# Performance work log

Hardware: AMD Instinct MI355X
Metric: run time of the kernel (lower is better)

## Reference

```python
import jax, jax.numpy as jnp
import numpy as np
import math

DIMS = [2048, 1024, 512, 4096]
NH, DK, DV = 16, 64, 64
BS = 8192
D_MODEL = NH * DK  # 1024


def setup_inputs() -> dict:
    key = jax.random.key(0)
    ks = jax.random.split(key, 3 * len(DIMS) + 5)
    inp = {"input_data": jax.random.normal(ks[0], (BS, sum(DIMS)), jnp.float32)}
    ki = 1
    for i, d in enumerate(DIMS):
        inp[f"wq{i}"] = jax.random.normal(ks[ki], (NH * DK, d), jnp.float32) * 0.02; ki += 1
        inp[f"wk{i}"] = jax.random.normal(ks[ki], (NH * DK, d), jnp.float32) * 0.02; ki += 1
        inp[f"wv{i}"] = jax.random.normal(ks[ki], (NH * DV, d), jnp.float32) * 0.02; ki += 1
    inp["fc_w"] = jax.random.normal(ks[ki], (NH * DV, NH * DV), jnp.float32) * 0.02; ki += 1
    inp["fc_b"] = jax.random.normal(ks[ki], (NH * DV,), jnp.float32) * 0.02; ki += 1
    inp["ln_g"] = jnp.ones((NH * DV,), jnp.float32)
    inp["ln_b"] = jnp.zeros((NH * DV,), jnp.float32)
    return inp


def _forward(input_data, wqs, wks, wvs, fc_w, fc_b, ln_g, ln_b):
    bs = input_data.shape[0]
    M = len(DIMS)
    offs = np.cumsum([0] + DIMS)
    # per-modality projections; stack into [bs, M, NH*D]
    xs = [input_data[:, offs[i]:offs[i + 1]] for i in range(M)]
    q = jnp.stack([x @ w.T for x, w in zip(xs, wqs)], axis=1)  # [bs, M, NH*DK]
    k = jnp.stack([x @ w.T for x, w in zip(xs, wks)], axis=1)
    v = jnp.stack([x @ w.T for x, w in zip(xs, wvs)], axis=1)  # [bs, M, NH*DV]
    residual = v  # v.transpose(1,2).view == original stacked v
    qh = q.reshape(bs, M, NH, DK).transpose(0, 2, 1, 3)  # [bs, NH, M, DK]
    kh = k.reshape(bs, M, NH, DK).transpose(0, 2, 1, 3)
    vh = v.reshape(bs, M, NH, DV).transpose(0, 2, 1, 3)
    scores = jnp.einsum('bhqd,bhkd->bhqk', qh, kh) / math.sqrt(DK)
    attn = jax.nn.softmax(scores, axis=-1)  # [bs, NH, M, M]
    ctx = jnp.einsum('bhqk,bhkd->bhqd', attn, vh)  # [bs, NH, M, DV]
    ctx = ctx.transpose(0, 2, 1, 3).reshape(bs, M, NH * DV)
    out = ctx @ fc_w.T + fc_b  # dropout is identity (p=0 / eval)
    out = out + residual
    mu = jnp.mean(out, axis=-1, keepdims=True)
    var = jnp.var(out, axis=-1, keepdims=True)
    out = (out - mu) / jnp.sqrt(var + 1e-6) * ln_g + ln_b
    return out, attn


def reference(input_data, wq0, wk0, wv0, wq1, wk1, wv1, wq2, wk2, wv2,
              wq3, wk3, wv3, fc_w, fc_b, ln_g, ln_b):
    wqs = [wq0, wq1, wq2, wq3]
    wks = [wk0, wk1, wk2, wk3]
    wvs = [wv0, wv1, wv2, wv3]
    return _forward(input_data, wqs, wks, wvs, fc_w, fc_b, ln_g, ln_b)
```

## Files before the change

### kernel.cpp

```cpp
#include <hip/hip_runtime.h>


typedef unsigned short u16;
typedef short short8 __attribute__((ext_vector_type(8)));
typedef float f32x4 __attribute__((ext_vector_type(4)));

__device__ __forceinline__ u16 f2bf(float f) {
  unsigned u = __builtin_bit_cast(unsigned, f);
  u += 0x7FFFu + ((u >> 16) & 1u);
  return (u16)(u >> 16);
}
__device__ __forceinline__ float bf2f(u16 s) {
  return __builtin_bit_cast(float, ((unsigned)s) << 16);
}

__device__ __forceinline__ void gload16(const u16* g, u16* l) {
  __builtin_amdgcn_global_load_lds(
      (const __attribute__((address_space(1))) void*)g,
      (__attribute__((address_space(3))) void*)l, 16, 0, 0);
}

#define CFENCE asm volatile("" ::: "memory")

struct CArgs {
  const float* src[14];
  unsigned long dst[14];
  int blk0[14];
  int n4[14];
};

__global__ __launch_bounds__(256) void convall(CArgs a, u16* __restrict__ wsb) {
  int blk = blockIdx.x;
  int s = 0;
#pragma unroll
  for (int i = 1; i < 14; ++i) s = (blk >= a.blk0[i]) ? i : s;
  int li = (blk - a.blk0[s]) * 256 + threadIdx.x;
  if (li < a.n4[s]) {
    float4 v = ((const float4*)a.src[s])[li];
    ushort4 o;
    o.x = f2bf(v.x); o.y = f2bf(v.y); o.z = f2bf(v.z); o.w = f2bf(v.w);
    ((ushort4*)(wsb + a.dst[s]))[li] = o;
  }
}

template <int MODE>
__global__ __launch_bounds__(512, 1)
void gemm8(const u16* __restrict__ Abase, int lda,
           const u16* __restrict__ Wbase, u16* __restrict__ Cq,
           float* __restrict__ Cf, const float* __restrict__ bias,
           const u16* __restrict__ resid) {
  __shared__ __align__(16) u16 lds[65536];

  const int tid = threadIdx.x;
  const int w = tid >> 6, lane = tid & 63;
  const int lr = lane & 15, lk = lane >> 4;
  const int wm = w >> 2, wn = w & 3;

  int K, nt, bx, by, coff;
  const u16 *A, *B;
  if (MODE == 0) {
    int seg = blockIdx.x / 384;
    int r = blockIdx.x % 384;
    r = (r & 7) * 48 + (r >> 3);
    bx = r % 12; by = r / 12;
    K = 4096 >> seg; nt = 128 >> seg;
    int xo, wo, mod;
    switch (seg) {
      case 0:  xo = 3584; wo = 11010048; mod = 3; break;
      case 1:  xo = 0;    wo = 0;        mod = 0; break;
      case 2:  xo = 2048; wo = 6291456;  mod = 1; break;
      default: xo = 3072; wo = 9437184;  mod = 2; break;
    }
    coff = mod * 3072;
    A = Abase + xo;
    B = Wbase + wo;
  } else {
    int r = (blockIdx.x & 7) * 64 + (blockIdx.x >> 3);
    bx = r & 3; by = r >> 2;
    K = 1024; nt = 32; coff = 0;
    A = Abase; B = Wbase;
  }
  const size_t brow = (size_t)by * 256;
  const int bcol = bx * 256;
  const u16* Ab = A + brow * (size_t)lda;
  const u16* Bb = B + (size_t)bcol * (size_t)K;

  const int stg_row = lane >> 2;
  const int stg_k = ((lane & 3) ^ ((lane >> 3) & 3)) * 8;
  const int fso = (lk ^ ((lr >> 1) & 3)) * 8;

  f32x4 acc[8][4];
#pragma unroll
  for (int i = 0; i < 8; ++i)
#pragma unroll
    for (int j = 0; j < 4; ++j) acc[i][j] = (f32x4){0.f, 0.f, 0.f, 0.f};

  auto stageA = [&](int p) {
    const int bb = (p & 3) * 16384;
    const int k0 = p * 32;
#pragma unroll
    for (int h = 0; h < 2; ++h)
      gload16(Ab + (size_t)(h * 128 + w * 16 + stg_row) * lda + k0 + stg_k,
              (u16*)&lds[bb + h * 4096 + w * 512]);
  };
  auto stageB = [&](int p) {
    const int bb = (p & 3) * 16384 + 8192;
    const int k0 = p * 32;
#pragma unroll
    for (int h = 0; h < 2; ++h)
      gload16(Bb + (size_t)(h * 128 + w * 16 + stg_row) * (size_t)K + k0 + stg_k,
              (u16*)&lds[bb + h * 4096 + w * 512]);
  };

  stageA(0); stageB(0);
  stageA(1); stageB(1);
  stageA(2); stageB(2);
  asm volatile("s_waitcnt vmcnt(8)" ::: "memory");
  __builtin_amdgcn_s_barrier();
  CFENCE;

#pragma unroll 1
  for (int t = 0; t < nt; ++t) {
    const int bb = (t & 3) * 16384;
    short8 af[4], bfr[4];
#pragma unroll
    for (int mi = 0; mi < 4; ++mi)
      af[mi] = *(const short8*)&lds[bb + (wm * 128 + mi * 16 + lr) * 32 + fso];
#pragma unroll
    for (int ni = 0; ni < 4; ++ni)
      bfr[ni] = *(const short8*)&lds[bb + 8192 + (wn * 64 + ni * 16 + lr) * 32 + fso];
    if (t + 3 < nt) stageA(t + 3);
    CFENCE;
    __builtin_amdgcn_s_barrier();
    CFENCE;
    __builtin_amdgcn_s_setprio(1);
#pragma unroll
    for (int mi = 0; mi < 4; ++mi)
#pragma unroll
      for (int ni = 0; ni < 4; ++ni)
        acc[mi][ni] = __builtin_amdgcn_mfma_f32_16x16x32_bf16(
            af[mi], bfr[ni], acc[mi][ni], 0, 0, 0);
    __builtin_amdgcn_s_setprio(0);
    CFENCE;
    __builtin_amdgcn_s_barrier();
    CFENCE;
    short8 ag[4];
#pragma unroll
    for (int mi = 0; mi < 4; ++mi)
      ag[mi] = *(const short8*)&lds[bb + (wm * 128 + (mi + 4) * 16 + lr) * 32 + fso];
    if (t + 3 < nt) stageB(t + 3);
    CFENCE;
    __builtin_amdgcn_s_barrier();
    CFENCE;
    __builtin_amdgcn_s_setprio(1);
#pragma unroll
    for (int mi = 0; mi < 4; ++mi)
#pragma unroll
      for (int ni = 0; ni < 4; ++ni)
        acc[mi + 4][ni] = __builtin_amdgcn_mfma_f32_16x16x32_bf16(
            ag[mi], bfr[ni], acc[mi + 4][ni], 0, 0, 0);
    __builtin_amdgcn_s_setprio(0);
    if (t + 1 < nt) {
      if (t + 3 < nt)      asm volatile("s_waitcnt vmcnt(8)" ::: "memory");
      else if (t + 2 < nt) asm volatile("s_waitcnt vmcnt(4)" ::: "memory");
      else                 asm volatile("s_waitcnt vmcnt(0)" ::: "memory");
      __builtin_amdgcn_s_barrier();
      CFENCE;
    }
  }

  if (MODE == 0) {
#pragma unroll
    for (int mi = 0; mi < 8; ++mi)
#pragma unroll
      for (int ni = 0; ni < 4; ++ni) {
        const int c = coff + bcol + wn * 64 + ni * 16 + lr;
#pragma unroll
        for (int j = 0; j < 4; ++j) {
          size_t r = brow + wm * 128 + mi * 16 + lk * 4 + j;
          Cq[r * 12288 + c] = f2bf(acc[mi][ni][j]);
        }
      }
  } else {
#pragma unroll
    for (int mi = 0; mi < 8; ++mi)
#pragma unroll
      for (int ni = 0; ni < 4; ++ni) {
        const int c = bcol + wn * 64 + ni * 16 + lr;
        const float bs = bias[c];
#pragma unroll
        for (int j = 0; j < 4; ++j) {
          size_t r = brow + wm * 128 + mi * 16 + lk * 4 + j;
          size_t ridx = (r >> 2) * 12288 + (r & 3) * 3072 + 2048 + c;
          Cf[r * 1024 + c] = acc[mi][ni][j] + bs + bf2f(resid[ridx]);
        }
      }
  }
}

__global__ __launch_bounds__(256) void attn_k(const u16* __restrict__ qkv,
                                              u16* __restrict__ ctxb,
                                              float* __restrict__ attn_out) {
  const int tid = threadIdx.x;
  const int l = tid & 63;
  const int wg = blockIdx.x * 4 + (tid >> 6);
  const int b = wg >> 2;
  const int h0 = (wg & 3) << 2;
  const size_t base = (size_t)b * 12288 + h0 * 64 + l * 4;

  float q[4][4], k[4][4], v[4][4];
#pragma unroll
  for (int m = 0; m < 4; ++m) {
    ushort4 uq = *(const ushort4*)(qkv + base + m * 3072);
    ushort4 uk = *(const ushort4*)(qkv + base + m * 3072 + 1024);
    ushort4 uv = *(const ushort4*)(qkv + base + m * 3072 + 2048);
    q[m][0] = bf2f(uq.x); q[m][1] = bf2f(uq.y); q[m][2] = bf2f(uq.z); q[m][3] = bf2f(uq.w);
    k[m][0] = bf2f(uk.x); k[m][1] = bf2f(uk.y); k[m][2] = bf2f(uk.z); k[m][3] = bf2f(uk.w);
    v[m][0] = bf2f(uv.x); v[m][1] = bf2f(uv.y); v[m][2] = bf2f(uv.z); v[m][3] = bf2f(uv.w);
  }

  float s[16];
#pragma unroll
  for (int i = 0; i < 4; ++i)
#pragma unroll
    for (int j = 0; j < 4; ++j) {
      float acc = q[i][0] * k[j][0];
      acc += q[i][1] * k[j][1];
      acc += q[i][2] * k[j][2];
      acc += q[i][3] * k[j][3];
      s[i * 4 + j] = acc;
    }
#pragma unroll
  for (int off = 1; off < 16; off <<= 1) {
#pragma unroll
    for (int t = 0; t < 16; ++t) s[t] += __shfl_xor(s[t], off);
  }

  float a[16];
#pragma unroll
  for (int i = 0; i < 4; ++i) {
    float s0 = s[i * 4 + 0] * 0.125f, s1 = s[i * 4 + 1] * 0.125f;
    float s2 = s[i * 4 + 2] * 0.125f, s3 = s[i * 4 + 3] * 0.125f;
    float m = fmaxf(fmaxf(s0, s1), fmaxf(s2, s3));
    float e0 = __expf(s0 - m), e1 = __expf(s1 - m);
    float e2 = __expf(s2 - m), e3 = __expf(s3 - m);
    float inv = 1.0f / (e0 + e1 + e2 + e3);
    a[i * 4 + 0] = e0 * inv; a[i * 4 + 1] = e1 * inv;
    a[i * 4 + 2] = e2 * inv; a[i * 4 + 3] = e3 * inv;
  }

#pragma unroll
  for (int i = 0; i < 4; ++i) {
    float c0 = a[i*4+0]*v[0][0] + a[i*4+1]*v[1][0] + a[i*4+2]*v[2][0] + a[i*4+3]*v[3][0];
    float c1 = a[i*4+0]*v[0][1] + a[i*4+1]*v[1][1] + a[i*4+2]*v[2][1] + a[i*4+3]*v[3][1];
    float c2 = a[i*4+0]*v[0][2] + a[i*4+1]*v[1][2] + a[i*4+2]*v[2][2] + a[i*4+3]*v[3][2];
    float c3 = a[i*4+0]*v[0][3] + a[i*4+1]*v[1][3] + a[i*4+2]*v[2][3] + a[i*4+3]*v[3][3];
    ushort4 o;
    o.x = f2bf(c0); o.y = f2bf(c1); o.z = f2bf(c2); o.w = f2bf(c3);
    *(ushort4*)(ctxb + (size_t)b * 4096 + i * 1024 + h0 * 64 + l * 4) = o;
  }

  int sel = l & 15;
  float val = a[0];
#pragma unroll
  for (int t = 1; t < 16; ++t) val = (sel == t) ? a[t] : val;
  attn_out[(size_t)b * 256 + h0 * 16 + l] = val;
}

__global__ __launch_bounds__(256) void ln_k(const float* __restrict__ pre,
                                            const float* __restrict__ g,
                                            const float* __restrict__ b,
                                            float* __restrict__ out) {
  int row = blockIdx.x;
  int tid = threadIdx.x;
  const float4 x = *(const float4*)(pre + (size_t)row * 1024 + tid * 4);
  float s = x.x + x.y + x.z + x.w;
  float s2 = x.x * x.x + x.y * x.y + x.z * x.z + x.w * x.w;
#pragma unroll
  for (int off = 32; off; off >>= 1) {
    s += __shfl_xor(s, off);
    s2 += __shfl_xor(s2, off);
  }
  __shared__ float r1[4], r2[4];
  int w = tid >> 6, lane = tid & 63;
  if (lane == 0) { r1[w] = s; r2[w] = s2; }
  __syncthreads();
  s = r1[0] + r1[1] + r1[2] + r1[3];
  s2 = r2[0] + r2[1] + r2[2] + r2[3];
  float mu = s * (1.0f / 1024.0f);
  float inv = rsqrtf(s2 * (1.0f / 1024.0f) - mu * mu + 1e-6f);
  float4 gv = *(const float4*)(g + tid * 4);
  float4 bv = *(const float4*)(b + tid * 4);
  float4 o;
  o.x = (x.x - mu) * inv * gv.x + bv.x;
  o.y = (x.y - mu) * inv * gv.y + bv.y;
  o.z = (x.z - mu) * inv * gv.z + bv.z;
  o.w = (x.w - mu) * inv * gv.w + bv.w;
  *(float4*)(out + (size_t)row * 1024 + tid * 4) = o;
}

extern "C" void kernel_launch(void* const* d_in, const int* in_sizes, int n_in,
                              void* d_out, int out_size, void* d_ws,
                              size_t ws_size, hipStream_t stream) {
  const float* fcb = (const float*)d_in[14];
  const float* lng = (const float*)d_in[15];
  const float* lnb = (const float*)d_in[16];

  u16* wsb = (u16*)d_ws;
  u16* xb = wsb;
  u16* wb = xb + 62914560;
  u16* qkv = wb + 24641536;
  u16* ctxb = qkv + 100663296;
  float* pre = (float*)d_ws;
  float* outp = (float*)d_out;
  float* attn_out = outp + 33554432;

  static const unsigned long woff[13] = {
      0,        2097152,  4194304,
      6291456,  7340032,  8388608,
      9437184,  9961472,  10485760,
      11010048, 15204352, 19398656,
      23592960};
  static const int wn4[13] = {524288, 524288, 524288, 262144, 262144, 262144,
                              131072, 131072, 131072, 1048576, 1048576, 1048576,
                              262144};

  CArgs ca;
  ca.src[0] = (const float*)d_in[0];
  ca.dst[0] = 0;
  ca.n4[0] = 62914560 / 4;
  ca.blk0[0] = 0;
  int nb = ca.n4[0] / 256;
  for (int i = 0; i < 13; ++i) {
    ca.src[i + 1] = (const float*)d_in[1 + i];
    ca.dst[i + 1] = 62914560ul + woff[i];
    ca.n4[i + 1] = wn4[i];
    ca.blk0[i + 1] = nb;
    nb += (wn4[i] + 255) / 256;
  }
  convall<<<dim3(nb), 256, 0, stream>>>(ca, wsb);

  gemm8<0><<<dim3(1536), 512, 0, stream>>>(xb, 7680, wb, qkv, nullptr, nullptr,
                                           nullptr);

  attn_k<<<dim3(8192), 256, 0, stream>>>(qkv, ctxb, attn_out);

  gemm8<1><<<dim3(512), 512, 0, stream>>>(ctxb, 1024, wb + 23592960, nullptr,
                                          pre, fcb, qkv);

  ln_k<<<dim3(32768), 256, 0, stream>>>(pre, lng, lnb, outp);
}
```

Measured before the change: 666.7 us.

## Raise GEMM occupancy, drop block swizzle, store pre-LN output as bf16

Sets launch bounds to two blocks per CU, reuses the A-fragment registers instead of a second array, removes the XCD-aware block index remapping, and makes the end-of-iteration barrier unconditional. The FC GEMM now writes its pre-LayerNorm sum as bf16 rather than fp32, and the LN kernel reads bf16, halving that intermediate traffic. The risks are register spills from the tighter occupancy bound, worse L2 locality without the swizzle, and lost precision in the LayerNorm input. With 128KB of LDS per block, two blocks may not actually fit per CU anyway.

```diff
diff --git a/kernel.cpp b/kernel.cpp
--- a/kernel.cpp
+++ b/kernel.cpp
@@ -44,10 +44,10 @@
 }
 
 template <int MODE>
-__global__ __launch_bounds__(512, 1)
+__global__ __launch_bounds__(512, 2)
 void gemm8(const u16* __restrict__ Abase, int lda,
            const u16* __restrict__ Wbase, u16* __restrict__ Cq,
-           float* __restrict__ Cf, const float* __restrict__ bias,
+           u16* __restrict__ Cpre, const float* __restrict__ bias,
            const u16* __restrict__ resid) {
   __shared__ __align__(16) u16 lds[65536];
 
@@ -61,7 +61,6 @@
   if (MODE == 0) {
     int seg = blockIdx.x / 384;
     int r = blockIdx.x % 384;
-    r = (r & 7) * 48 + (r >> 3);
     bx = r % 12; by = r / 12;
     K = 4096 >> seg; nt = 128 >> seg;
     int xo, wo, mod;
@@ -75,8 +74,7 @@
     A = Abase + xo;
     B = Wbase + wo;
   } else {
-    int r = (blockIdx.x & 7) * 64 + (blockIdx.x >> 3);
-    bx = r & 3; by = r >> 2;
+    bx = blockIdx.x & 3; by = blockIdx.x >> 2;
     K = 1024; nt = 32; coff = 0;
     A = Abase; B = Wbase;
   }
@@ -85,8 +83,8 @@
   const u16* Ab = A + brow * (size_t)lda;
   const u16* Bb = B + (size_t)bcol * (size_t)K;
 
+  const int stg_k = ((lane & 3) ^ ((lane >> 3) & 3)) * 8;
   const int stg_row = lane >> 2;
-  const int stg_k = ((lane & 3) ^ ((lane >> 3) & 3)) * 8;
   const int fso = (lk ^ ((lr >> 1) & 3)) * 8;
 
   f32x4 acc[8][4];
@@ -144,10 +142,9 @@
     CFENCE;
     __builtin_amdgcn_s_barrier();
     CFENCE;
-    short8 ag[4];
 #pragma unroll
     for (int mi = 0; mi < 4; ++mi)
-      ag[mi] = *(const short8*)&lds[bb + (wm * 128 + (mi + 4) * 16 + lr) * 32 + fso];
+      af[mi] = *(const short8*)&lds[bb + (wm * 128 + (4 + mi) * 16 + lr) * 32 + fso];
     if (t + 3 < nt) stageB(t + 3);
     CFENCE;
     __builtin_amdgcn_s_barrier();
@@ -158,15 +155,17 @@
 #pragma unroll
       for (int ni = 0; ni < 4; ++ni)
         acc[mi + 4][ni] = __builtin_amdgcn_mfma_f32_16x16x32_bf16(
-            ag[mi], bfr[ni], acc[mi + 4][ni], 0, 0, 0);
+            af[mi], bfr[ni], acc[mi + 4][ni], 0, 0, 0);
     __builtin_amdgcn_s_setprio(0);
+    CFENCE;
     if (t + 1 < nt) {
       if (t + 3 < nt)      asm volatile("s_waitcnt vmcnt(8)" ::: "memory");
       else if (t + 2 < nt) asm volatile("s_waitcnt vmcnt(4)" ::: "memory");
       else                 asm volatile("s_waitcnt vmcnt(0)" ::: "memory");
-      __builtin_amdgcn_s_barrier();
-      CFENCE;
     }
+    CFENCE;
+    __builtin_amdgcn_s_barrier();
+    CFENCE;
   }
 
   if (MODE == 0) {
@@ -192,7 +191,7 @@
         for (int j = 0; j < 4; ++j) {
           size_t r = brow + wm * 128 + mi * 16 + lk * 4 + j;
           size_t ridx = (r >> 2) * 12288 + (r & 3) * 3072 + 2048 + c;
-          Cf[r * 1024 + c] = acc[mi][ni][j] + bs + bf2f(resid[ridx]);
+          Cpre[r * 1024 + c] = f2bf(acc[mi][ni][j] + bs + bf2f(resid[ridx]));
         }
       }
   }
@@ -267,15 +266,16 @@
   attn_out[(size_t)b * 256 + h0 * 16 + l] = val;
 }
 
-__global__ __launch_bounds__(256) void ln_k(const float* __restrict__ pre,
+__global__ __launch_bounds__(256) void ln_k(const u16* __restrict__ pre,
                                             const float* __restrict__ g,
                                             const float* __restrict__ b,
                                             float* __restrict__ out) {
   int row = blockIdx.x;
   int tid = threadIdx.x;
-  const float4 x = *(const float4*)(pre + (size_t)row * 1024 + tid * 4);
-  float s = x.x + x.y + x.z + x.w;
-  float s2 = x.x * x.x + x.y * x.y + x.z * x.z + x.w * x.w;
+  ushort4 u = *(const ushort4*)(pre + (size_t)row * 1024 + tid * 4);
+  float x0 = bf2f(u.x), x1 = bf2f(u.y), x2 = bf2f(u.z), x3 = bf2f(u.w);
+  float s = x0 + x1 + x2 + x3;
+  float s2 = x0 * x0 + x1 * x1 + x2 * x2 + x3 * x3;
 #pragma unroll
   for (int off = 32; off; off >>= 1) {
     s += __shfl_xor(s, off);
@@ -292,10 +292,10 @@
   float4 gv = *(const float4*)(g + tid * 4);
   float4 bv = *(const float4*)(b + tid * 4);
   float4 o;
-  o.x = (x.x - mu) * inv * gv.x + bv.x;
-  o.y = (x.y - mu) * inv * gv.y + bv.y;
-  o.z = (x.z - mu) * inv * gv.z + bv.z;
-  o.w = (x.w - mu) * inv * gv.w + bv.w;
+  o.x = (x0 - mu) * inv * gv.x + bv.x;
+  o.y = (x1 - mu) * inv * gv.y + bv.y;
+  o.z = (x2 - mu) * inv * gv.z + bv.z;
+  o.w = (x3 - mu) * inv * gv.w + bv.w;
   *(float4*)(out + (size_t)row * 1024 + tid * 4) = o;
 }
 
@@ -311,7 +311,7 @@
   u16* wb = xb + 62914560;
   u16* qkv = wb + 24641536;
   u16* ctxb = qkv + 100663296;
-  float* pre = (float*)d_ws;
+  u16* pre = wsb;
   float* outp = (float*)d_out;
   float* attn_out = outp + 33554432;
 
```

After: 652.2 us (median of 2 runs). -2.2%, faster.
